# Kernel tuning notes

Measured on AMD Instinct MI355X. Metric: run time of the kernel, lower is better.

## Reference

```python
import jax, jax.numpy as jnp
import numpy as np

NEIGH_RADIUS = 1
NEIGH_DILATION = 1
NB_ITER = 3
GROUP_NB = 4
SOFTMAX_FACT = 1.0
EPS = 1e-8


def _directions():
    # matches computeNeighborsCoord: (x, y) pairs, row-major over y then x, center removed
    r = NEIGH_RADIUS
    return [(x * NEIGH_DILATION, y * NEIGH_DILATION)
            for y in range(-r, r + 1) for x in range(-r, r + 1)
            if not (x == 0 and y == 0)]


def _shift(feat, dx, dy):
    # out[..., i, j] = feat[..., i+dy, j+dx], zero outside the image; mask marks valid positions
    H, W = feat.shape[2], feat.shape[3]
    shifted = jnp.roll(feat, shift=(-dy, -dx), axis=(2, 3))
    vy = (np.arange(H) + dy >= 0) & (np.arange(H) + dy < H)
    vx = (np.arange(W) + dx >= 0) & (np.arange(W) + dx < W)
    mask = jnp.asarray(np.outer(vy, vx).astype(np.float32))[None, None]  # [1,1,H,W]
    return shifted * mask, mask


def _cossim(a, b):
    # channel-wise cosine similarity -> [B,1,H,W]
    num = jnp.sum(a * b, axis=1, keepdims=True)
    den = jnp.sqrt(jnp.sum(a * a, axis=1, keepdims=True)) * jnp.sqrt(jnp.sum(b * b, axis=1, keepdims=True))
    return num / jnp.maximum(den, EPS)


def _total_sim(feat, dirs):
    # mask-normalized mean cosine similarity with the 8 neighbors -> [B,1,H,W]
    num = 0.0
    cnt = 0.0
    for dx, dy in dirs:
        fs, m = _shift(feat, dx, dy)
        num = num + _cossim(feat, fs) * m
        cnt = cnt + m
    return num / cnt


def setup_inputs() -> dict:
    key = jax.random.key(0)
    features = jax.random.normal(key, (8, 32, 256, 256), dtype=jnp.float32)
    return {"features": features}


def reference(features):
    dirs = _directions()
    sim_maps = [_total_sim(features, dirs)]
    for _ in range(NB_ITER):
        sims = []
        fshifts = []
        for dx, dy in dirs:
            fs, m = _shift(features, dx, dy)
            sims.append(_cossim(features, fs) * m)  # masked sim, zeros at invalid positions
            fshifts.append(fs)                       # already masked shift
        all_sim = jax.nn.softmax(SOFTMAX_FACT * jnp.concatenate(sims, axis=1), axis=1)  # [B,8,H,W]
        new_feat = sum(all_sim[:, i:i + 1] * fshifts[i] for i in range(len(dirs)))       # [B,C,H,W]
        sim_maps.append(_total_sim(features, dirs))  # NOTE: pre-update features, as in original
        new_feat = new_feat / jnp.sum(all_sim, axis=1, keepdims=True)  # == conv2d with ones(1,8,1,1)
        features = new_feat
    out = jnp.concatenate(sim_maps, axis=1)  # [B, nbIter+1, H, W]
    B, T, H, W = out.shape
    out = out.reshape(B // GROUP_NB, GROUP_NB, T, H, W).mean(axis=1)
    return out
```

## Files before the change

kernel.cpp:

```cpp
#include <hip/hip_runtime.h>
#include <hip/hip_fp16.h>

#define HH 256
#define WW 256
#define CC 32
#define HWSZ (HH * WW)
#define IMGSZ (CC * HWSZ)
#define NIMG 8
#define EPSV 1e-8f
#define NCH (CC / 2)

__device__ __forceinline__ void acc_pass1(const float v[3][6],
                                          float sq[3][6], float dotv[8][4])
{
#pragma unroll
    for (int r = 0; r < 3; ++r)
#pragma unroll
        for (int j = 0; j < 6; ++j) sq[r][j] = fmaf(v[r][j], v[r][j], sq[r][j]);
    int d = 0;
#pragma unroll
    for (int dyi = 0; dyi < 3; ++dyi)
#pragma unroll
        for (int dxi = 0; dxi < 3; ++dxi) {
            if (dyi == 1 && dxi == 1) continue;
#pragma unroll
            for (int i = 0; i < 4; ++i)
                dotv[d][i] = fmaf(v[1][i + 1], v[dyi][i + dxi], dotv[d][i]);
            ++d;
        }
}

__device__ __forceinline__ void acc_pass2(const float v[3][6],
                                          const float w[8][4], float o[4])
{
    int d = 0;
#pragma unroll
    for (int dyi = 0; dyi < 3; ++dyi)
#pragma unroll
        for (int dxi = 0; dxi < 3; ++dxi) {
            if (dyi == 1 && dxi == 1) continue;
#pragma unroll
            for (int i = 0; i < 4; ++i)
                o[i] = fmaf(w[d][i], v[dyi][i + dxi], o[i]);
            ++d;
        }
}

__device__ __forceinline__ void gload16(const void* g, void* l)
{
    __builtin_amdgcn_global_load_lds(
        (const __attribute__((address_space(1))) void*)g,
        (__attribute__((address_space(3))) void*)l, 16, 0, 0);
}

__device__ __forceinline__ float cvtlo(unsigned u)
{ return __half2float(__ushort_as_half((unsigned short)(u & 0xffffu))); }
__device__ __forceinline__ float cvthi(unsigned u)
{ return __half2float(__ushort_as_half((unsigned short)(u >> 16))); }
__device__ __forceinline__ float cvt16(unsigned short u)
{ return __half2float(__ushort_as_half(u)); }
__device__ __forceinline__ unsigned pkh(float a, float b)
{
    return (unsigned)__half_as_ushort(__float2half_rn(a)) |
           ((unsigned)__half_as_ushort(__float2half_rn(b)) << 16);
}

#define WAITB(VM) { asm volatile("s_waitcnt vmcnt(" #VM ")" ::: "memory"); \
                    __builtin_amdgcn_s_barrier(); }


#define STAGE(SLOT) { \
    const int ch_ = (SLOT) & 15; \
    const int bo_ = ((SLOT) % 5) * 8192; \
    gload16(gsrc0 + (size_t)ch_ * HWSZ,        ldst0 + bo_); \
    gload16(gsrc0 + (size_t)(ch_ + 16) * HWSZ, ldst0 + bo_ + 4096); }

#define LOADV(G, VV) { \
    const char* sp_ = slabb + ((G) % 5) * 8192; \
    _Pragma("unroll") \
    for (int r_ = 0; r_ < 3; ++r_) { \
        float4 m_ = *(const float4*)(sp_ + bM + r_ * 1024); \
        float e_ = 0.f; \
        if (edge) e_ = *(const float*)(sp_ + bE + r_ * 1024); \
        const float lu_ = __shfl_up(m_.w, 1); \
        const float rd_ = __shfl_down(m_.x, 1); \
        const bool ok_ = rowok[r_]; \
        VV[r_][0] = (ok_ && xl) ? ((tx == 0)  ? e_ : lu_) : 0.f; \
        VV[r_][1] = ok_ ? m_.x : 0.f; \
        VV[r_][2] = ok_ ? m_.y : 0.f; \
        VV[r_][3] = ok_ ? m_.z : 0.f; \
        VV[r_][4] = ok_ ? m_.w : 0.f; \
        VV[r_][5] = (ok_ && xr) ? ((tx == 31) ? e_ : rd_) : 0.f; \
    } }

#define P2STORE(G) { \
    float v[3][6]; LOADV(G, v) \
    float o[4] = { 0.f, 0.f, 0.f, 0.f }; acc_pass2(v, w, o); \
    uint2 ov; ov.x = pkh(o[0], o[1]); ov.y = pkh(o[2], o[3]); \
    *reinterpret_cast<uint2*>(outp + ((G) & 15) * HWSZ) = ov; }

template <bool YEDGE>
__device__ __forceinline__ void step1_body(const float* __restrict__ F,
                                           unsigned short* __restrict__ Fn,
                                           float* __restrict__ simout,
                                           char* slabb, int b, int rowblk, int tid)
{
    const int wave = tid >> 6;
    const int lane = tid & 63;
    const int half = lane >> 5;
    const int tx   = lane & 31;
    const int y0   = rowblk * 2;
    const int y    = y0 + (wave >> 1);
    const int x0   = (wave & 1) * 128 + (tx << 2);
    const int c0   = half * NCH;

    const bool ym = YEDGE ? (y > 0) : true;
    const bool yp = YEDGE ? (y < HH - 1) : true;
    const bool xl = x0 > 0, xr = x0 < WW - 4;
    const bool rowok[3] = { ym, true, yp };
    const bool colok[6] = { xl, true, true, true, true, xr };

    const float* Fb = F + (size_t)b * IMGSZ;
    int arow = y0 - 1 + wave;
    if (YEDGE) arow = arow < 0 ? 0 : (arow > HH - 1 ? HH - 1 : arow);
    const float* gsrc0 = Fb + arow * WW + (lane << 2);
    char* ldst0 = slabb + wave * 1024;

    const int rbase = half * 4096 + (wave >> 1) * 1024;
    const int bM = rbase + x0 * 4;
    const int bL = rbase + (xl ? x0 * 4 - 4 : 0);
    const int bR = rbase + (xr ? x0 * 4 + 16 : 1020);
    const bool edge = (tx == 0) || (tx == 31);
    const int bE = (tx == 31) ? bR : bL;

    float sq[3][6];
    float dotv[8][4];
#pragma unroll
    for (int r = 0; r < 3; ++r)
#pragma unroll
        for (int j = 0; j < 6; ++j) sq[r][j] = 0.f;
#pragma unroll
    for (int d = 0; d < 8; ++d)
#pragma unroll
        for (int i = 0; i < 4; ++i) dotv[d][i] = 0.f;

    STAGE(0) STAGE(1) STAGE(2) STAGE(3)

#pragma unroll 1
    for (int g = 0; g < 16; ++g) {
        WAITB(6)
        STAGE(g + 4)
        float v[3][6];
        LOADV(g, v)
        acc_pass1(v, sq, dotv);
    }

#pragma unroll
    for (int r = 0; r < 3; ++r)
#pragma unroll
        for (int j = 0; j < 6; ++j) sq[r][j] += __shfl_xor(sq[r][j], 32);
#pragma unroll
    for (int d = 0; d < 8; ++d)
#pragma unroll
        for (int i = 0; i < 4; ++i) dotv[d][i] += __shfl_xor(dotv[d][i], 32);

    float nrm[3][6];
#pragma unroll
    for (int r = 0; r < 3; ++r)
#pragma unroll
        for (int j = 0; j < 6; ++j) nrm[r][j] = __builtin_amdgcn_sqrtf(sq[r][j]);

    float w[8][4];
    float simarr[4];
#pragma unroll
    for (int i = 0; i < 4; ++i) {
        float s[8];
        const float cn = nrm[1][i + 1];
        float tot = 0.f, cnt = 0.f;
        int d = 0;
#pragma unroll
        for (int dyi = 0; dyi < 3; ++dyi)
#pragma unroll
            for (int dxi = 0; dxi < 3; ++dxi) {
                if (dyi == 1 && dxi == 1) continue;
                const bool m = rowok[dyi] && colok[i + dxi];
                const float den = fmaxf(cn * nrm[dyi][i + dxi], EPSV);
                const float cs = dotv[d][i] * __builtin_amdgcn_rcpf(den);
                s[d] = m ? cs : 0.f;
                tot += s[d];
                cnt += m ? 1.f : 0.f;
                ++d;
            }
        simarr[i] = tot * __builtin_amdgcn_rcpf(cnt);
        {
            float mx = s[0];
#pragma unroll
            for (int d2 = 1; d2 < 8; ++d2) mx = fmaxf(mx, s[d2]);
            float wsum = 0.f;
#pragma unroll
            for (int d2 = 0; d2 < 8; ++d2) { w[d2][i] = __expf(s[d2] - mx); wsum += w[d2][i]; }
            const float inv = __builtin_amdgcn_rcpf(wsum);
#pragma unroll
            for (int d2 = 0; d2 < 8; ++d2) w[d2][i] *= inv;
        }
    }
    if (half == 0) {
        float4 simv = { simarr[0], simarr[1], simarr[2], simarr[3] };
        *reinterpret_cast<float4*>(simout + b * HWSZ + y * WW + x0) = simv;
    }

    {
        unsigned short* outp = Fn + (size_t)b * IMGSZ + (size_t)c0 * HWSZ + y * WW + x0;
        { WAITB(7)  STAGE(20) P2STORE(16) }
        { WAITB(8)  STAGE(21) P2STORE(17) }
        { WAITB(9)  STAGE(22) P2STORE(18) }
#pragma unroll 1
        for (int g = 19; g < 28; ++g) {
            WAITB(10)
            STAGE(g + 4)
            P2STORE(g)
        }
        { WAITB(10) P2STORE(28) }
        { WAITB(8)  P2STORE(29) }
        { WAITB(6)  P2STORE(30) }
        { WAITB(4)  P2STORE(31) }
    }
}

__global__ __launch_bounds__(256, 4) void step1_kernel(const float* __restrict__ F,
                                                       unsigned short* __restrict__ Fn,
                                                       float* __restrict__ simout)
{
    const int linear = blockIdx.y * (HH / 2) + blockIdx.x;
    const int remap  = (linear & 7) * 128 + (linear >> 3);
    const int b      = remap >> 7;
    const int rowblk = remap & 127;

    __shared__ float4 slab4[2560];

    if (rowblk != 0 && rowblk != 127)
        step1_body<false>(F, Fn, simout, (char*)slab4, b, rowblk, threadIdx.x);
    else
        step1_body<true>(F, Fn, simout, (char*)slab4, b, rowblk, threadIdx.x);
}


#define STAGE_P(P) { \
    const int ps_ = ((P) % 3) * 8192; \
    gload16(gsrcH + (size_t)(2 * ((P) & 7)     + halfS * 16) * HWSZ, ldstH + ps_); \
    gload16(gsrcH + (size_t)(2 * ((P) & 7) + 1 + halfS * 16) * HWSZ, ldstH + ps_ + 4096); }

#define LOADV_H(SB, VV) { \
    const char* sp_ = slabb + (SB); \
    _Pragma("unroll") \
    for (int r_ = 0; r_ < 3; ++r_) { \
        uint2 b_ = *(const uint2*)(sp_ + bMH + r_ * 512); \
        unsigned short lo_ = *(const unsigned short*)(sp_ + bLo + r_ * 512); \
        unsigned short hi_ = *(const unsigned short*)(sp_ + bHi + r_ * 512); \
        const bool ok_ = rowok[r_]; \
        VV[r_][0] = (ok_ && xl) ? cvt16(lo_) : 0.f; \
        VV[r_][1] = ok_ ? cvtlo(b_.x) : 0.f; \
        VV[r_][2] = ok_ ? cvthi(b_.x) : 0.f; \
        VV[r_][3] = ok_ ? cvtlo(b_.y) : 0.f; \
        VV[r_][4] = ok_ ? cvthi(b_.y) : 0.f; \
        VV[r_][5] = (ok_ && xr) ? cvt16(hi_) : 0.f; \
    } }

template <bool YEDGE, bool COMPUTE_NEXT>
__device__ __forceinline__ void steph_body(const unsigned short* __restrict__ F,
                                           unsigned short* __restrict__ Fn,
                                           float* __restrict__ simout,
                                           char* slabb, int b, int rowblk, int tid)
{
    const int wave = tid >> 6;
    const int lane = tid & 63;
    const int half = lane >> 5;
    const int tx   = lane & 31;
    const int y0   = rowblk * 2;
    const int y    = y0 + (wave >> 1);
    const int x0   = (wave & 1) * 128 + (tx << 2);
    const int c0   = half * NCH;

    const bool ym = YEDGE ? (y > 0) : true;
    const bool yp = YEDGE ? (y < HH - 1) : true;
    const bool xl = x0 > 0, xr = x0 < WW - 4;
    const bool rowok[3] = { ym, true, yp };
    const bool colok[6] = { xl, true, true, true, true, xr };

    const unsigned short* Fb = F + (size_t)b * IMGSZ;

    const int halfS = wave >> 1;
    const int rp    = wave & 1;
    int srow = y0 - 1 + 2 * rp;
    int dsh  = 0;
    if (YEDGE) {
        if (srow < 0)               { srow = 0;      dsh = 512;  }
        else if (srow + 1 > HH - 1) { srow = HH - 2; dsh = -512; }
    }
    const unsigned short* gsrcH = Fb + srow * WW + lane * 8;
    char* ldstH = slabb + halfS * 2048 + rp * 1024 + dsh;

    const int bMH = half * 2048 + (wave >> 1) * 512 + x0 * 2;
    const int bLo = bMH + (xl ? -2 : 0);
    const int bHi = bMH + (xr ?  8 : 0);

    float sq[3][6];
    float dotv[8][4];
#pragma unroll
    for (int r = 0; r < 3; ++r)
#pragma unroll
        for (int j = 0; j < 6; ++j) sq[r][j] = 0.f;
#pragma unroll
    for (int d = 0; d < 8; ++d)
#pragma unroll
        for (int i = 0; i < 4; ++i) dotv[d][i] = 0.f;

    STAGE_P(0) STAGE_P(1)

#pragma unroll 1
    for (int p = 0; p < (COMPUTE_NEXT ? 8 : 6); ++p) {
        WAITB(2)
        const int sb = (p % 3) * 8192;
        { float v[3][6]; LOADV_H(sb, v)        acc_pass1(v, sq, dotv); }
        { float v[3][6]; LOADV_H(sb + 4096, v) acc_pass1(v, sq, dotv); }
        STAGE_P(p + 2)
    }
    if (!COMPUTE_NEXT) {
        { WAITB(2) const int sb = 0;
          float v[3][6]; LOADV_H(sb, v)        acc_pass1(v, sq, dotv);
          { float u[3][6]; LOADV_H(sb + 4096, u) acc_pass1(u, sq, dotv); } }
        { WAITB(0) const int sb = 8192;
          float v[3][6]; LOADV_H(sb, v)        acc_pass1(v, sq, dotv);
          { float u[3][6]; LOADV_H(sb + 4096, u) acc_pass1(u, sq, dotv); } }
    }

#pragma unroll
    for (int r = 0; r < 3; ++r)
#pragma unroll
        for (int j = 0; j < 6; ++j) sq[r][j] += __shfl_xor(sq[r][j], 32);
#pragma unroll
    for (int d = 0; d < 8; ++d)
#pragma unroll
        for (int i = 0; i < 4; ++i) dotv[d][i] += __shfl_xor(dotv[d][i], 32);

    float nrm[3][6];
#pragma unroll
    for (int r = 0; r < 3; ++r)
#pragma unroll
        for (int j = 0; j < 6; ++j) nrm[r][j] = __builtin_amdgcn_sqrtf(sq[r][j]);

    float w[8][4];
    float simarr[4];
#pragma unroll
    for (int i = 0; i < 4; ++i) {
        float s[8];
        const float cn = nrm[1][i + 1];
        float tot = 0.f, cnt = 0.f;
        int d = 0;
#pragma unroll
        for (int dyi = 0; dyi < 3; ++dyi)
#pragma unroll
            for (int dxi = 0; dxi < 3; ++dxi) {
                if (dyi == 1 && dxi == 1) continue;
                const bool m = rowok[dyi] && colok[i + dxi];
                const float den = fmaxf(cn * nrm[dyi][i + dxi], EPSV);
                const float cs = dotv[d][i] * __builtin_amdgcn_rcpf(den);
                s[d] = m ? cs : 0.f;
                tot += s[d];
                cnt += m ? 1.f : 0.f;
                ++d;
            }
        simarr[i] = tot * __builtin_amdgcn_rcpf(cnt);
        if (COMPUTE_NEXT) {
            float mx = s[0];
#pragma unroll
            for (int d2 = 1; d2 < 8; ++d2) mx = fmaxf(mx, s[d2]);
            float wsum = 0.f;
#pragma unroll
            for (int d2 = 0; d2 < 8; ++d2) { w[d2][i] = __expf(s[d2] - mx); wsum += w[d2][i]; }
            const float inv = __builtin_amdgcn_rcpf(wsum);
#pragma unroll
            for (int d2 = 0; d2 < 8; ++d2) w[d2][i] *= inv;
        }
    }
    if (half == 0) {
        float4 simv = { simarr[0], simarr[1], simarr[2], simarr[3] };
        *reinterpret_cast<float4*>(simout + b * HWSZ + y * WW + x0) = simv;
    }

    if (COMPUTE_NEXT) {
        unsigned short* outp = Fn + (size_t)b * IMGSZ + (size_t)c0 * HWSZ + y * WW + x0;

#define PASS2_PAIR(P) { \
            const int sb_ = ((P) % 3) * 8192; \
            const int ch_ = 2 * ((P) & 7); \
            { float v[3][6]; LOADV_H(sb_, v) \
              float o[4] = { 0.f, 0.f, 0.f, 0.f }; acc_pass2(v, w, o); \
              uint2 ov; ov.x = pkh(o[0], o[1]); ov.y = pkh(o[2], o[3]); \
              *reinterpret_cast<uint2*>(outp + ch_ * HWSZ) = ov; } \
            { float v[3][6]; LOADV_H(sb_ + 4096, v) \
              float o[4] = { 0.f, 0.f, 0.f, 0.f }; acc_pass2(v, w, o); \
              uint2 ov; ov.x = pkh(o[0], o[1]); ov.y = pkh(o[2], o[3]); \
              *reinterpret_cast<uint2*>(outp + (ch_ + 1) * HWSZ) = ov; } }

        { WAITB(3) PASS2_PAIR(8) STAGE_P(10) }
#pragma unroll 1
        for (int p = 9; p < 14; ++p) {
            WAITB(4)
            PASS2_PAIR(p)
            STAGE_P(p + 2)
        }
        { WAITB(4) PASS2_PAIR(14) }
        { WAITB(2) PASS2_PAIR(15) }
#undef PASS2_PAIR
    }
}

template <bool COMPUTE_NEXT>
__global__ __launch_bounds__(256, 4) void steph_kernel(const unsigned short* __restrict__ F,
                                                       unsigned short* __restrict__ Fn,
                                                       float* __restrict__ simout)
{
    const int linear = blockIdx.y * (HH / 2) + blockIdx.x;
    const int remap  = (linear & 7) * 128 + (linear >> 3);
    const int b      = remap >> 7;
    const int rowblk = remap & 127;

    __shared__ float4 slabH[1536];

    if (rowblk != 0 && rowblk != 127)
        steph_body<false, COMPUTE_NEXT>(F, Fn, simout, (char*)slabH, b, rowblk, threadIdx.x);
    else
        steph_body<true,  COMPUTE_NEXT>(F, Fn, simout, (char*)slabH, b, rowblk, threadIdx.x);
}

__global__ __launch_bounds__(256) void reduce_kernel(const float* __restrict__ sims,
                                                     float* __restrict__ out)
{
    const int idx = blockIdx.x * blockDim.x + threadIdx.x;
    const int p4 = idx & (HWSZ / 4 - 1);
    const int t  = (idx >> 14) & 3;
    const int g  = idx >> 16;
    const int tt = (t <= 1) ? 0 : (t - 1);
    const float4* s = reinterpret_cast<const float4*>(sims) +
                      (size_t)(tt * NIMG + g * 4) * (HWSZ / 4) + p4;
    float4 a = s[0];
    float4 b = s[HWSZ / 4];
    float4 c = s[2 * (HWSZ / 4)];
    float4 d = s[3 * (HWSZ / 4)];
    float4 o;
    o.x = 0.25f * (a.x + b.x + c.x + d.x);
    o.y = 0.25f * (a.y + b.y + c.y + d.y);
    o.z = 0.25f * (a.z + b.z + c.z + d.z);
    o.w = 0.25f * (a.w + b.w + c.w + d.w);
    reinterpret_cast<float4*>(out)[idx] = o;
}

extern "C" void kernel_launch(void* const* d_in, const int* in_sizes, int n_in,
                              void* d_out, int out_size, void* d_ws, size_t ws_size,
                              hipStream_t stream)
{
    const float* F0 = (const float*)d_in[0];
    unsigned short* F1h = (unsigned short*)d_ws;
    unsigned short* F2h = F1h + (size_t)NIMG * IMGSZ;
    float* sims = (float*)(F2h + (size_t)NIMG * IMGSZ);

    dim3 block(256);
    dim3 grid(HH / 2, NIMG);

    hipLaunchKernelGGL(step1_kernel,          grid, block, 0, stream, F0, F1h, sims);
    hipLaunchKernelGGL((steph_kernel<true>),  grid, block, 0, stream, F1h, F2h, sims + (size_t)NIMG * HWSZ);
    hipLaunchKernelGGL((steph_kernel<false>), grid, block, 0, stream, F2h, nullptr, sims + (size_t)2 * NIMG * HWSZ);

    hipLaunchKernelGGL(reduce_kernel, dim3((2 * 4 * HWSZ / 4) / 256), block, 0, stream,
                       sims, (float*)d_out);
}
```

Baseline: 88.71 us.

## Stage fp32 input as fp16 in LDS via register prefetch in step1

The first-step kernel no longer copies fp32 rows straight into LDS through a 5-slot async global-to-LDS ring. It now loads float4s into registers, converts them to packed fp16, and writes them into a 3-slot fp16 LDS ring laid out like the later half-precision steps. That layout lets it reuse the LOADV_H path and processes two channels per stage, which should cut LDS footprint (24KB vs 40KB) and LDS read traffic. The cost is extra registers for three in-flight prefetch sets, and fp16 rounding of the first-step input, which changes numerics of the similarity computation.

```diff
diff --git a/kernel.cpp b/kernel.cpp
--- a/kernel.cpp
+++ b/kernel.cpp
@@ -68,187 +68,8 @@
 #define WAITB(VM) { asm volatile("s_waitcnt vmcnt(" #VM ")" ::: "memory"); \
                     __builtin_amdgcn_s_barrier(); }
 
-
-#define STAGE(SLOT) { \
-    const int ch_ = (SLOT) & 15; \
-    const int bo_ = ((SLOT) % 5) * 8192; \
-    gload16(gsrc0 + (size_t)ch_ * HWSZ,        ldst0 + bo_); \
-    gload16(gsrc0 + (size_t)(ch_ + 16) * HWSZ, ldst0 + bo_ + 4096); }
-
-#define LOADV(G, VV) { \
-    const char* sp_ = slabb + ((G) % 5) * 8192; \
-    _Pragma("unroll") \
-    for (int r_ = 0; r_ < 3; ++r_) { \
-        float4 m_ = *(const float4*)(sp_ + bM + r_ * 1024); \
-        float e_ = 0.f; \
-        if (edge) e_ = *(const float*)(sp_ + bE + r_ * 1024); \
-        const float lu_ = __shfl_up(m_.w, 1); \
-        const float rd_ = __shfl_down(m_.x, 1); \
-        const bool ok_ = rowok[r_]; \
-        VV[r_][0] = (ok_ && xl) ? ((tx == 0)  ? e_ : lu_) : 0.f; \
-        VV[r_][1] = ok_ ? m_.x : 0.f; \
-        VV[r_][2] = ok_ ? m_.y : 0.f; \
-        VV[r_][3] = ok_ ? m_.z : 0.f; \
-        VV[r_][4] = ok_ ? m_.w : 0.f; \
-        VV[r_][5] = (ok_ && xr) ? ((tx == 31) ? e_ : rd_) : 0.f; \
-    } }
-
-#define P2STORE(G) { \
-    float v[3][6]; LOADV(G, v) \
-    float o[4] = { 0.f, 0.f, 0.f, 0.f }; acc_pass2(v, w, o); \
-    uint2 ov; ov.x = pkh(o[0], o[1]); ov.y = pkh(o[2], o[3]); \
-    *reinterpret_cast<uint2*>(outp + ((G) & 15) * HWSZ) = ov; }
-
-template <bool YEDGE>
-__device__ __forceinline__ void step1_body(const float* __restrict__ F,
-                                           unsigned short* __restrict__ Fn,
-                                           float* __restrict__ simout,
-                                           char* slabb, int b, int rowblk, int tid)
-{
-    const int wave = tid >> 6;
-    const int lane = tid & 63;
-    const int half = lane >> 5;
-    const int tx   = lane & 31;
-    const int y0   = rowblk * 2;
-    const int y    = y0 + (wave >> 1);
-    const int x0   = (wave & 1) * 128 + (tx << 2);
-    const int c0   = half * NCH;
-
-    const bool ym = YEDGE ? (y > 0) : true;
-    const bool yp = YEDGE ? (y < HH - 1) : true;
-    const bool xl = x0 > 0, xr = x0 < WW - 4;
-    const bool rowok[3] = { ym, true, yp };
-    const bool colok[6] = { xl, true, true, true, true, xr };
-
-    const float* Fb = F + (size_t)b * IMGSZ;
-    int arow = y0 - 1 + wave;
-    if (YEDGE) arow = arow < 0 ? 0 : (arow > HH - 1 ? HH - 1 : arow);
-    const float* gsrc0 = Fb + arow * WW + (lane << 2);
-    char* ldst0 = slabb + wave * 1024;
-
-    const int rbase = half * 4096 + (wave >> 1) * 1024;
-    const int bM = rbase + x0 * 4;
-    const int bL = rbase + (xl ? x0 * 4 - 4 : 0);
-    const int bR = rbase + (xr ? x0 * 4 + 16 : 1020);
-    const bool edge = (tx == 0) || (tx == 31);
-    const int bE = (tx == 31) ? bR : bL;
-
-    float sq[3][6];
-    float dotv[8][4];
-#pragma unroll
-    for (int r = 0; r < 3; ++r)
-#pragma unroll
-        for (int j = 0; j < 6; ++j) sq[r][j] = 0.f;
-#pragma unroll
-    for (int d = 0; d < 8; ++d)
-#pragma unroll
-        for (int i = 0; i < 4; ++i) dotv[d][i] = 0.f;
-
-    STAGE(0) STAGE(1) STAGE(2) STAGE(3)
-
-#pragma unroll 1
-    for (int g = 0; g < 16; ++g) {
-        WAITB(6)
-        STAGE(g + 4)
-        float v[3][6];
-        LOADV(g, v)
-        acc_pass1(v, sq, dotv);
-    }
-
-#pragma unroll
-    for (int r = 0; r < 3; ++r)
-#pragma unroll
-        for (int j = 0; j < 6; ++j) sq[r][j] += __shfl_xor(sq[r][j], 32);
-#pragma unroll
-    for (int d = 0; d < 8; ++d)
-#pragma unroll
-        for (int i = 0; i < 4; ++i) dotv[d][i] += __shfl_xor(dotv[d][i], 32);
-
-    float nrm[3][6];
-#pragma unroll
-    for (int r = 0; r < 3; ++r)
-#pragma unroll
-        for (int j = 0; j < 6; ++j) nrm[r][j] = __builtin_amdgcn_sqrtf(sq[r][j]);
-
-    float w[8][4];
-    float simarr[4];
-#pragma unroll
-    for (int i = 0; i < 4; ++i) {
-        float s[8];
-        const float cn = nrm[1][i + 1];
-        float tot = 0.f, cnt = 0.f;
-        int d = 0;
-#pragma unroll
-        for (int dyi = 0; dyi < 3; ++dyi)
-#pragma unroll
-            for (int dxi = 0; dxi < 3; ++dxi) {
-                if (dyi == 1 && dxi == 1) continue;
-                const bool m = rowok[dyi] && colok[i + dxi];
-                const float den = fmaxf(cn * nrm[dyi][i + dxi], EPSV);
-                const float cs = dotv[d][i] * __builtin_amdgcn_rcpf(den);
-                s[d] = m ? cs : 0.f;
-                tot += s[d];
-                cnt += m ? 1.f : 0.f;
-                ++d;
-            }
-        simarr[i] = tot * __builtin_amdgcn_rcpf(cnt);
-        {
-            float mx = s[0];
-#pragma unroll
-            for (int d2 = 1; d2 < 8; ++d2) mx = fmaxf(mx, s[d2]);
-            float wsum = 0.f;
-#pragma unroll
-            for (int d2 = 0; d2 < 8; ++d2) { w[d2][i] = __expf(s[d2] - mx); wsum += w[d2][i]; }
-            const float inv = __builtin_amdgcn_rcpf(wsum);
-#pragma unroll
-            for (int d2 = 0; d2 < 8; ++d2) w[d2][i] *= inv;
-        }
-    }
-    if (half == 0) {
-        float4 simv = { simarr[0], simarr[1], simarr[2], simarr[3] };
-        *reinterpret_cast<float4*>(simout + b * HWSZ + y * WW + x0) = simv;
-    }
-
-    {
-        unsigned short* outp = Fn + (size_t)b * IMGSZ + (size_t)c0 * HWSZ + y * WW + x0;
-        { WAITB(7)  STAGE(20) P2STORE(16) }
-        { WAITB(8)  STAGE(21) P2STORE(17) }
-        { WAITB(9)  STAGE(22) P2STORE(18) }
-#pragma unroll 1
-        for (int g = 19; g < 28; ++g) {
-            WAITB(10)
-            STAGE(g + 4)
-            P2STORE(g)
-        }
-        { WAITB(10) P2STORE(28) }
-        { WAITB(8)  P2STORE(29) }
-        { WAITB(6)  P2STORE(30) }
-        { WAITB(4)  P2STORE(31) }
-    }
-}
-
-__global__ __launch_bounds__(256, 4) void step1_kernel(const float* __restrict__ F,
-                                                       unsigned short* __restrict__ Fn,
-                                                       float* __restrict__ simout)
-{
-    const int linear = blockIdx.y * (HH / 2) + blockIdx.x;
-    const int remap  = (linear & 7) * 128 + (linear >> 3);
-    const int b      = remap >> 7;
-    const int rowblk = remap & 127;
-
-    __shared__ float4 slab4[2560];
-
-    if (rowblk != 0 && rowblk != 127)
-        step1_body<false>(F, Fn, simout, (char*)slab4, b, rowblk, threadIdx.x);
-    else
-        step1_body<true>(F, Fn, simout, (char*)slab4, b, rowblk, threadIdx.x);
-}
-
-
-#define STAGE_P(P) { \
-    const int ps_ = ((P) % 3) * 8192; \
-    gload16(gsrcH + (size_t)(2 * ((P) & 7)     + halfS * 16) * HWSZ, ldstH + ps_); \
-    gload16(gsrcH + (size_t)(2 * ((P) & 7) + 1 + halfS * 16) * HWSZ, ldstH + ps_ + 4096); }
+#define LGB { asm volatile("s_waitcnt lgkmcnt(0)" ::: "memory"); \
+              __builtin_amdgcn_s_barrier(); }
 
 #define LOADV_H(SB, VV) { \
     const char* sp_ = slabb + (SB); \
@@ -265,6 +86,193 @@
         VV[r_][4] = ok_ ? cvthi(b_.y) : 0.f; \
         VV[r_][5] = (ok_ && xr) ? cvt16(hi_) : 0.f; \
     } }
+
+
+#define ISS(L, P) { \
+    const float* c0_ = gsrcF + (size_t)(2 * ((P) & 7) + halfS * 16) * HWSZ; \
+    const float* c1_ = c0_ + HWSZ; \
+    q##L##a = *(const float4*)(c0_);       q##L##b = *(const float4*)(c0_ + 128); \
+    q##L##c = *(const float4*)(c1_);       q##L##d = *(const float4*)(c1_ + 128); }
+
+#define WRT(L, P) { \
+    char* wb_ = wrbase + ((P) % 3) * 8192; \
+    uint2 u0_, u1_, u2_, u3_; \
+    u0_.x = pkh(q##L##a.x, q##L##a.y); u0_.y = pkh(q##L##a.z, q##L##a.w); \
+    u1_.x = pkh(q##L##b.x, q##L##b.y); u1_.y = pkh(q##L##b.z, q##L##b.w); \
+    u2_.x = pkh(q##L##c.x, q##L##c.y); u2_.y = pkh(q##L##c.z, q##L##c.w); \
+    u3_.x = pkh(q##L##d.x, q##L##d.y); u3_.y = pkh(q##L##d.z, q##L##d.w); \
+    *(uint2*)(wb_)              = u0_; \
+    *(uint2*)(wb_ + 256)        = u1_; \
+    *(uint2*)(wb_ + 4096)       = u2_; \
+    *(uint2*)(wb_ + 4096 + 256) = u3_; }
+
+#define CS1(SLOT) { \
+    float v_[3][6]; LOADV_H((SLOT) * 8192, v_)        acc_pass1(v_, sq, dotv); \
+    float u_[3][6]; LOADV_H((SLOT) * 8192 + 4096, u_) acc_pass1(u_, sq, dotv); }
+
+#define CS2(SLOT, CH) { \
+    { float v_[3][6]; LOADV_H((SLOT) * 8192, v_) \
+      float o_[4] = { 0.f, 0.f, 0.f, 0.f }; acc_pass2(v_, w, o_); \
+      uint2 ov_; ov_.x = pkh(o_[0], o_[1]); ov_.y = pkh(o_[2], o_[3]); \
+      *(uint2*)(outp + (CH) * HWSZ) = ov_; } \
+    { float v_[3][6]; LOADV_H((SLOT) * 8192 + 4096, v_) \
+      float o_[4] = { 0.f, 0.f, 0.f, 0.f }; acc_pass2(v_, w, o_); \
+      uint2 ov_; ov_.x = pkh(o_[0], o_[1]); ov_.y = pkh(o_[2], o_[3]); \
+      *(uint2*)(outp + ((CH) + 1) * HWSZ) = ov_; } }
+
+template <bool YEDGE>
+__device__ __forceinline__ void step1_body(const float* __restrict__ F,
+                                           unsigned short* __restrict__ Fn,
+                                           float* __restrict__ simout,
+                                           char* slabb, int b, int rowblk, int tid)
+{
+    const int wave = tid >> 6;
+    const int lane = tid & 63;
+    const int half = lane >> 5;
+    const int tx   = lane & 31;
+    const int y0   = rowblk * 2;
+    const int y    = y0 + (wave >> 1);
+    const int x0   = (wave & 1) * 128 + (tx << 2);
+    const int c0   = half * NCH;
+
+    const bool ym = YEDGE ? (y > 0) : true;
+    const bool yp = YEDGE ? (y < HH - 1) : true;
+    const bool xl = x0 > 0, xr = x0 < WW - 4;
+    const bool rowok[3] = { ym, true, yp };
+    const bool colok[6] = { xl, true, true, true, true, xr };
+
+    const float* Fb = F + (size_t)b * IMGSZ;
+
+    const int halfS = wave >> 1;
+    const int rp    = wave & 1;
+    int srow = y0 - 1 + 2 * rp;
+    int dsh  = 0;
+    if (YEDGE) {
+        if (srow < 0)               { srow = 0;      dsh = 512;  }
+        else if (srow + 1 > HH - 1) { srow = HH - 2; dsh = -512; }
+    }
+    const float* gsrcF = Fb + (size_t)(srow + (lane >> 5)) * WW + (lane & 31) * 4;
+    char* wrbase = slabb + halfS * 2048 + rp * 1024 + dsh
+                 + (lane >> 5) * 512 + (lane & 31) * 8;
+
+    const int bMH = half * 2048 + (wave >> 1) * 512 + x0 * 2;
+    const int bLo = bMH + (xl ? -2 : 0);
+    const int bHi = bMH + (xr ?  8 : 0);
+
+    float4 qAa, qAb, qAc, qAd;
+    float4 qBa, qBb, qBc, qBd;
+    float4 qCa, qCb, qCc, qCd;
+
+    float sq[3][6];
+    float dotv[8][4];
+#pragma unroll
+    for (int r = 0; r < 3; ++r)
+#pragma unroll
+        for (int j = 0; j < 6; ++j) sq[r][j] = 0.f;
+#pragma unroll
+    for (int d = 0; d < 8; ++d)
+#pragma unroll
+        for (int i = 0; i < 4; ++i) dotv[d][i] = 0.f;
+
+    ISS(A, 0) ISS(B, 1) ISS(C, 2)
+    WRT(A, 0) WRT(B, 1) LGB
+
+    CS1(0) ISS(A, 3)  WRT(C, 2) LGB
+    CS1(1) ISS(B, 4)  WRT(A, 3) LGB
+    CS1(2) ISS(C, 5)  WRT(B, 4) LGB
+    CS1(0) ISS(A, 6)  WRT(C, 5) LGB
+    CS1(1) ISS(B, 7)  WRT(A, 6) LGB
+    CS1(2) ISS(C, 8)  WRT(B, 7) LGB
+    CS1(0) ISS(A, 9)  WRT(C, 8) LGB
+    CS1(1) ISS(B, 10) WRT(A, 9) LGB
+
+#pragma unroll
+    for (int r = 0; r < 3; ++r)
+#pragma unroll
+        for (int j = 0; j < 6; ++j) sq[r][j] += __shfl_xor(sq[r][j], 32);
+#pragma unroll
+    for (int d = 0; d < 8; ++d)
+#pragma unroll
+        for (int i = 0; i < 4; ++i) dotv[d][i] += __shfl_xor(dotv[d][i], 32);
+
+    float nrm[3][6];
+#pragma unroll
+    for (int r = 0; r < 3; ++r)
+#pragma unroll
+        for (int j = 0; j < 6; ++j) nrm[r][j] = __builtin_amdgcn_sqrtf(sq[r][j]);
+
+    float w[8][4];
+    float simarr[4];
+#pragma unroll
+    for (int i = 0; i < 4; ++i) {
+        float s[8];
+        const float cn = nrm[1][i + 1];
+        float tot = 0.f, cnt = 0.f;
+        int d = 0;
+#pragma unroll
+        for (int dyi = 0; dyi < 3; ++dyi)
+#pragma unroll
+            for (int dxi = 0; dxi < 3; ++dxi) {
+                if (dyi == 1 && dxi == 1) continue;
+                const bool m = rowok[dyi] && colok[i + dxi];
+                const float den = fmaxf(cn * nrm[dyi][i + dxi], EPSV);
+                const float cs = dotv[d][i] * __builtin_amdgcn_rcpf(den);
+                s[d] = m ? cs : 0.f;
+                tot += s[d];
+                cnt += m ? 1.f : 0.f;
+                ++d;
+            }
+        simarr[i] = tot * __builtin_amdgcn_rcpf(cnt);
+        {
+            float mx = s[0];
+#pragma unroll
+            for (int d2 = 1; d2 < 8; ++d2) mx = fmaxf(mx, s[d2]);
+            float wsum = 0.f;
+#pragma unroll
+            for (int d2 = 0; d2 < 8; ++d2) { w[d2][i] = __expf(s[d2] - mx); wsum += w[d2][i]; }
+            const float inv = __builtin_amdgcn_rcpf(wsum);
+#pragma unroll
+            for (int d2 = 0; d2 < 8; ++d2) w[d2][i] *= inv;
+        }
+    }
+    if (half == 0) {
+        float4 simv = { simarr[0], simarr[1], simarr[2], simarr[3] };
+        *reinterpret_cast<float4*>(simout + b * HWSZ + y * WW + x0) = simv;
+    }
+
+    unsigned short* outp = Fn + (size_t)b * IMGSZ + (size_t)c0 * HWSZ + y * WW + x0;
+    CS2(2, 0)  ISS(C, 11) WRT(B, 10) LGB
+    CS2(0, 2)  ISS(A, 12) WRT(C, 11) LGB
+    CS2(1, 4)  ISS(B, 13) WRT(A, 12) LGB
+    CS2(2, 6)  ISS(C, 14) WRT(B, 13) LGB
+    CS2(0, 8)  ISS(A, 15) WRT(C, 14) LGB
+    CS2(1, 10)            WRT(A, 15) LGB
+    CS2(2, 12)
+    CS2(0, 14)
+}
+
+__global__ __launch_bounds__(256, 4) void step1_kernel(const float* __restrict__ F,
+                                                       unsigned short* __restrict__ Fn,
+                                                       float* __restrict__ simout)
+{
+    const int linear = blockIdx.y * (HH / 2) + blockIdx.x;
+    const int remap  = (linear & 7) * 128 + (linear >> 3);
+    const int b      = remap >> 7;
+    const int rowblk = remap & 127;
+
+    __shared__ float4 slabS[1536];
+
+    if (rowblk != 0 && rowblk != 127)
+        step1_body<false>(F, Fn, simout, (char*)slabS, b, rowblk, threadIdx.x);
+    else
+        step1_body<true>(F, Fn, simout, (char*)slabS, b, rowblk, threadIdx.x);
+}
+
+
+#define STAGE_P(P) { \
+    const int ps_ = ((P) % 3) * 8192; \
+    gload16(gsrcH + (size_t)(2 * ((P) & 7)     + halfS * 16) * HWSZ, ldstH + ps_); \
+    gload16(gsrcH + (size_t)(2 * ((P) & 7) + 1 + halfS * 16) * HWSZ, ldstH + ps_ + 4096); }
 
 template <bool YEDGE, bool COMPUTE_NEXT>
 __device__ __forceinline__ void steph_body(const unsigned short* __restrict__ F,
```

Result: slower. 184.0 us (+107.4%).
